# Optimization experiments

Measured on AMD Instinct MI355X. Metric: run time of the kernel, lower is better.

The kernel has to match this reference:

```python
import jax, jax.numpy as jnp
import numpy as np

B, L, D = 2, 4096, 768
H, HD = 12, 64
EPS = 1e-6


def setup_inputs() -> dict:
    key = jax.random.key(0)
    ks = jax.random.split(key, 5)
    x = jax.random.normal(ks[0], (B, L, D), dtype=jnp.float32)
    # realistic rope tables
    inv_freq = 1.0 / (10000.0 ** (np.arange(0, HD, 2, dtype=np.float32) / HD))
    t = np.arange(L, dtype=np.float32)
    freqs = np.outer(t, inv_freq)  # (L, HD/2)
    emb = np.concatenate([freqs, freqs], axis=-1)  # (L, HD)
    rope_cos = jnp.asarray(np.cos(emb))
    rope_sin = jnp.asarray(np.sin(emb))
    Wqkv = jax.random.normal(ks[1], (3 * D, D), dtype=jnp.float32) * (1.0 / np.sqrt(D))
    Wout = jax.random.normal(ks[2], (D, D), dtype=jnp.float32) * (1.0 / np.sqrt(D))
    q_norm_w = jnp.ones((HD,), dtype=jnp.float32)
    k_norm_w = jnp.ones((HD,), dtype=jnp.float32)
    return {"x": x, "rope_cos": rope_cos, "rope_sin": rope_sin,
            "Wqkv": Wqkv, "Wout": Wout,
            "q_norm_w": q_norm_w, "k_norm_w": k_norm_w}


def _rms_norm(x, w):
    # x: (..., HD); computed in float32 like the torch module
    norm = jax.lax.rsqrt(jnp.mean(jnp.square(x.astype(jnp.float32)), axis=-1, keepdims=True) + EPS)
    return (x.astype(jnp.float32) * norm).astype(x.dtype) * w


def _rotate_half(x):
    x1, x2 = jnp.split(x, 2, axis=-1)
    return jnp.concatenate([-x2, x1], axis=-1)


def reference(x, rope_cos, rope_sin, Wqkv, Wout, q_norm_w, k_norm_w):
    b, l, d = x.shape
    # fused QKV projection (Linear with no bias): x @ Wqkv.T
    qkv = jnp.einsum('bld,ed->ble', x, Wqkv).reshape(b, l, 3, H, HD)
    q, k, v = qkv[:, :, 0], qkv[:, :, 1], qkv[:, :, 2]  # (B, L, H, HD)
    q = jnp.transpose(q, (0, 2, 1, 3))  # (B, H, L, HD)
    k = jnp.transpose(k, (0, 2, 1, 3))
    v = jnp.transpose(v, (0, 2, 1, 3))
    # per-head RMSNorm on q and k
    q = _rms_norm(q, q_norm_w)
    k = _rms_norm(k, k_norm_w)
    # RoPE: cos/sin (L, HD) broadcast over (B, H)
    cos = rope_cos[None, None, :, :]
    sin = rope_sin[None, None, :, :]
    q = q * cos + _rotate_half(q) * sin
    k = k * cos + _rotate_half(k) * sin
    # scaled dot product attention (no mask)
    scale = 1.0 / jnp.sqrt(jnp.asarray(HD, dtype=q.dtype))
    scores = jnp.einsum('bhqd,bhkd->bhqk', q, k) * scale  # (B, H, L, L)
    attn = jax.nn.softmax(scores, axis=-1)
    out = jnp.einsum('bhqk,bhkd->bhqd', attn, v)  # (B, H, L, HD)
    out = jnp.transpose(out, (0, 2, 1, 3)).reshape(b, l, d)
    return jnp.einsum('bld,ed->ble', out, Wout)
```

## Files before the change

### kernel.cpp

```cpp
#include <hip/hip_runtime.h>
#include <hip/hip_bf16.h>

typedef float f32x4 __attribute__((ext_vector_type(4)));
typedef float f32x16 __attribute__((ext_vector_type(16)));
typedef short bf16x8 __attribute__((ext_vector_type(8)));
typedef unsigned short ushort8_t __attribute__((ext_vector_type(8)));

#define L_SEQ 4096
#define DMODEL 768
#define NHEAD 12
#define HDIM 64
#define QSCALE (0.125f * 1.44269504f)

__device__ __forceinline__ unsigned short f2bf(float f) {
    __hip_bfloat16 h = __float2bfloat16(f);
    return *reinterpret_cast<unsigned short*>(&h);
}

__device__ __forceinline__ unsigned pack2bf(float a, float b) {
    return (unsigned)f2bf(a) | ((unsigned)f2bf(b) << 16);
}

__device__ __forceinline__ void gload16(const void* g, void* l) {
    __builtin_amdgcn_global_load_lds(
        (const __attribute__((address_space(1))) unsigned int*)g,
        (__attribute__((address_space(3))) unsigned int*)l, 16, 0, 0);
}

__global__ __launch_bounds__(256) void cvt3_f32_bf16(
    const float* __restrict__ a, unsigned short* __restrict__ oa, int na,
    const float* __restrict__ bsrc, unsigned short* __restrict__ ob, int nb,
    const float* __restrict__ csrc, unsigned short* __restrict__ oc, int nc)
{
    int i = (blockIdx.x * 256 + threadIdx.x) * 4;
    const float* in; unsigned short* out;
    if (i < na) { in = a; out = oa; }
    else if (i < na + nb) { in = bsrc; out = ob; i -= na; }
    else if (i < na + nb + nc) { in = csrc; out = oc; i -= na + nb; }
    else return;
    float4 v = *reinterpret_cast<const float4*>(in + i);
    ushort4 o;
    o.x = f2bf(v.x); o.y = f2bf(v.y); o.z = f2bf(v.z); o.w = f2bf(v.w);
    *reinterpret_cast<ushort4*>(out + i) = o;
}

#define BM 128
#define BN 128
#define BKK 64

__global__ __launch_bounds__(256) void gemm_qkv_fused(
    const unsigned short* __restrict__ A, const unsigned short* __restrict__ Bt,
    const float* __restrict__ cosb, const float* __restrict__ sinb,
    const float* __restrict__ qw, const float* __restrict__ kw,
    unsigned short* __restrict__ Qb, unsigned short* __restrict__ Kb,
    unsigned short* __restrict__ Vt)
{
    __shared__ union SM {
        struct { unsigned short As[BM][BKK]; unsigned short Bs[BN][BKK]; } st;
        unsigned short ep[4][64][72];
    } sm;

    const int K = DMODEL;
    const int tid  = threadIdx.x;
    const int lane = tid & 63;
    const int wid  = tid >> 6;
    const int r = lane & 15, g = lane >> 4;
    const int wr = wid >> 1, wc = wid & 1;
    const int m0 = blockIdx.y * BM;
    const int n0 = blockIdx.x * BN;

    f32x4 acc[4][4];
    for (int i = 0; i < 4; ++i)
        for (int j = 0; j < 4; ++j)
            acc[i][j] = (f32x4){0.f, 0.f, 0.f, 0.f};

    for (int kt = 0; kt < K; kt += BKK) {
        __syncthreads();
        for (int p = 0; p < 4; ++p) {
            int idx = wid * 64 + p * 256 + lane;
            int row = idx >> 3;
            int ch  = (idx & 7) * 8;
            gload16(&A[(size_t)(m0 + row) * K + kt + ch],
                    (char*)sm.st.As + (size_t)(wid * 64 + p * 256) * 16);
            gload16(&Bt[(size_t)(n0 + row) * K + kt + ch],
                    (char*)sm.st.Bs + (size_t)(wid * 64 + p * 256) * 16);
        }
        __syncthreads();
        for (int k0 = 0; k0 < BKK; k0 += 32) {
            bf16x8 a[4], b[4];
            for (int i = 0; i < 4; ++i)
                a[i] = *reinterpret_cast<const bf16x8*>(&sm.st.As[wr * 64 + i * 16 + r][k0 + 8 * g]);
            for (int j = 0; j < 4; ++j)
                b[j] = *reinterpret_cast<const bf16x8*>(&sm.st.Bs[wc * 64 + j * 16 + r][k0 + 8 * g]);
            for (int i = 0; i < 4; ++i)
                for (int j = 0; j < 4; ++j)
                    acc[i][j] = __builtin_amdgcn_mfma_f32_16x16x32_bf16(a[i], b[j], acc[i][j], 0, 0, 0);
        }
    }

    __syncthreads();

    const int e0  = n0 + wc * 64;
    const int sec = e0 / DMODEL;
    const int h   = (e0 % DMODEL) / HDIM;
    const int row0 = m0 + wr * 64;
    const int b   = row0 >> 12;
    const int l0  = row0 & (L_SEQ - 1);
    unsigned short (*ep)[72] = sm.ep[wid];

    if (sec < 2) {
        const float* nw = (sec == 0) ? qw : kw;
        float wv[4];
        for (int j = 0; j < 4; ++j) wv[j] = nw[j * 16 + r];
        for (int i = 0; i < 4; ++i) {
            for (int t = 0; t < 4; ++t) {
                float ss = acc[i][0][t] * acc[i][0][t] + acc[i][1][t] * acc[i][1][t]
                         + acc[i][2][t] * acc[i][2][t] + acc[i][3][t] * acc[i][3][t];
                ss += __shfl_xor(ss, 1);
                ss += __shfl_xor(ss, 2);
                ss += __shfl_xor(ss, 4);
                ss += __shfl_xor(ss, 8);
                float inv = rsqrtf(ss * (1.f / 64.f) + 1e-6f);
                int lr = i * 16 + 4 * g + t;
                int l  = l0 + lr;
                float qn[4];
                for (int j = 0; j < 4; ++j) qn[j] = acc[i][j][t] * inv * wv[j];
                for (int j = 0; j < 4; ++j) {
                    int d = j * 16 + r;
                    float c = cosb[l * HDIM + d], s = sinb[l * HDIM + d];
                    float sgn = (j < 2) ? -1.f : 1.f;
                    float res = qn[j] * c + sgn * qn[j ^ 2] * s;
                    if (sec == 0) res *= QSCALE;
                    ep[lr][d] = f2bf(res);
                }
            }
        }
        unsigned short* dst = ((sec == 0) ? Qb : Kb)
            + ((size_t)(b * NHEAD + h) * L_SEQ + l0) * HDIM;
        for (int it = 0; it < 8; ++it) {
            int idx = it * 64 + lane;
            int lr = idx >> 3, ch = (idx & 7) * 8;
            ushort8_t v = *reinterpret_cast<const ushort8_t*>(&ep[lr][ch]);
            *reinterpret_cast<ushort8_t*>(&dst[(size_t)lr * HDIM + ch]) = v;
        }
    } else {
        for (int i = 0; i < 4; ++i)
            for (int t = 0; t < 4; ++t) {
                int lr = i * 16 + 4 * g + t;
                for (int j = 0; j < 4; ++j)
                    ep[j * 16 + r][lr] = f2bf(acc[i][j][t]);
            }
        unsigned short* dst = Vt + ((size_t)(b * NHEAD + h) * HDIM) * L_SEQ + l0;
        for (int it = 0; it < 8; ++it) {
            int idx = it * 64 + lane;
            int d = idx >> 3, ch = (idx & 7) * 8;
            ushort8_t v = *reinterpret_cast<const ushort8_t*>(&ep[d][ch]);
            *reinterpret_cast<ushort8_t*>(&dst[(size_t)d * L_SEQ + ch]) = v;
        }
    }
}

__global__ __launch_bounds__(256) void gemm_bf16_nt(
    const unsigned short* __restrict__ A, const unsigned short* __restrict__ Bt,
    float* __restrict__ C, int M, int N, int K)
{
    __shared__ unsigned short As[BM][BKK];
    __shared__ unsigned short Bs[BN][BKK];
    const int tid  = threadIdx.x;
    const int lane = tid & 63;
    const int wid  = tid >> 6;
    const int r = lane & 15, g = lane >> 4;
    const int wr = wid >> 1, wc = wid & 1;
    const int m0 = blockIdx.y * BM;
    const int n0 = blockIdx.x * BN;

    f32x4 acc[4][4];
    for (int i = 0; i < 4; ++i)
        for (int j = 0; j < 4; ++j)
            acc[i][j] = (f32x4){0.f, 0.f, 0.f, 0.f};

    for (int kt = 0; kt < K; kt += BKK) {
        __syncthreads();
        for (int p = 0; p < 4; ++p) {
            int idx = wid * 64 + p * 256 + lane;
            int row = idx >> 3;
            int ch  = (idx & 7) * 8;
            gload16(&A[(size_t)(m0 + row) * K + kt + ch],
                    (char*)As + (size_t)(wid * 64 + p * 256) * 16);
            gload16(&Bt[(size_t)(n0 + row) * K + kt + ch],
                    (char*)Bs + (size_t)(wid * 64 + p * 256) * 16);
        }
        __syncthreads();
        for (int k0 = 0; k0 < BKK; k0 += 32) {
            bf16x8 a[4], b[4];
            for (int i = 0; i < 4; ++i)
                a[i] = *reinterpret_cast<const bf16x8*>(&As[wr * 64 + i * 16 + r][k0 + 8 * g]);
            for (int j = 0; j < 4; ++j)
                b[j] = *reinterpret_cast<const bf16x8*>(&Bs[wc * 64 + j * 16 + r][k0 + 8 * g]);
            for (int i = 0; i < 4; ++i)
                for (int j = 0; j < 4; ++j)
                    acc[i][j] = __builtin_amdgcn_mfma_f32_16x16x32_bf16(a[i], b[j], acc[i][j], 0, 0, 0);
        }
    }
    for (int i = 0; i < 4; ++i)
        for (int j = 0; j < 4; ++j)
            for (int t = 0; t < 4; ++t) {
                int row = m0 + wr * 64 + i * 16 + 4 * g + t;
                int col = n0 + wc * 64 + j * 16 + r;
                C[(size_t)row * N + col] = acc[i][j][t];
            }
}

__global__ __launch_bounds__(256, 3) void flashattn(
    const unsigned short* __restrict__ Qb, const unsigned short* __restrict__ Kb,
    const unsigned short* __restrict__ Vt, unsigned short* __restrict__ aob)
{
    __shared__ unsigned short Ksm[2][64 * 64];
    __shared__ unsigned short Vsm[2][64 * 64];

    const int lin = blockIdx.x;
    const int bh = (lin & 7) + 8 * (lin >> 8);
    const int qblk = (lin >> 3) & 31;
    const int b = bh / NHEAD, h = bh % NHEAD;
    const int tid = threadIdx.x;
    const int wid = tid >> 6, lane = tid & 63;
    const int l31 = lane & 31, half = lane >> 5;
    const int q0 = qblk * 128 + wid * 32;

    bf16x8 qf[4];
    {
        const unsigned short* Qp = Qb + ((size_t)bh * L_SEQ + q0 + l31) * HDIM + 8 * half;
        for (int dt = 0; dt < 4; ++dt)
            qf[dt] = *reinterpret_cast<const bf16x8*>(Qp + dt * 16);
    }

    bf16x8 onesf;
    for (int e = 0; e < 8; ++e) onesf[e] = (l31 == 0) ? (short)0x3F80 : (short)0;

    const unsigned short* Kbase = Kb + (size_t)bh * L_SEQ * HDIM;
    const unsigned short* Vbase = Vt + (size_t)bh * HDIM * L_SEQ;

    const int idx0 = tid, idx1 = tid + 256;
    const int row0 = idx0 >> 3, row1 = idx1 >> 3;
    const int c0 = ((idx0 & 7) * 16) ^ ((row0 & 7) << 4);
    const int c1 = ((idx1 & 7) * 16) ^ ((row1 & 7) << 4);
    const char* kp0 = (const char*)(Kbase + (size_t)row0 * HDIM) + c0;
    const char* kp1 = (const char*)(Kbase + (size_t)row1 * HDIM) + c1;
    const char* vp0 = (const char*)(Vbase + (size_t)row0 * L_SEQ) + c0;
    const char* vp1 = (const char*)(Vbase + (size_t)row1 * L_SEQ) + c1;

    f32x16 o0, o1, o_l, sA0, sA1, sB0, sB1;
    for (int e = 0; e < 16; ++e) {
        o0[e] = 0.f; o1[e] = 0.f; o_l[e] = 0.f;
        sA0[e] = 0.f; sA1[e] = 0.f; sB0[e] = 0.f; sB1[e] = 0.f;
    }

    auto stageK = [&](int buf, int t) {
        size_t off = (size_t)t * (64 * HDIM * 2);
        gload16(kp0 + off, (char*)Ksm[buf] + wid * 1024);
        gload16(kp1 + off, (char*)Ksm[buf] + wid * 1024 + 4096);
    };
    auto stageV = [&](int buf, int t) {
        size_t off = (size_t)t * 128;
        gload16(vp0 + off, (char*)Vsm[buf] + wid * 1024);
        gload16(vp1 + off, (char*)Vsm[buf] + wid * 1024 + 4096);
    };

    auto qk = [&](f32x16& s0, f32x16& s1, const unsigned short* Kbuf) {
        const char* rp0 = (const char*)Kbuf + l31 * 128;
        const char* rp1 = rp0 + 32 * 128;
        const int sw = (l31 & 7) << 4;
        for (int dt = 0; dt < 4; ++dt) {
            int co = (dt * 32 + half * 16) ^ sw;
            bf16x8 kf0 = *reinterpret_cast<const bf16x8*>(rp0 + co);
            bf16x8 kf1 = *reinterpret_cast<const bf16x8*>(rp1 + co);
            s0 = __builtin_amdgcn_mfma_f32_32x32x16_bf16(kf0, qf[dt], s0, 0, 0, 0);
            s1 = __builtin_amdgcn_mfma_f32_32x32x16_bf16(kf1, qf[dt], s1, 0, 0, 0);
        }
    };

    auto softmax_pa = [&](f32x16& s0, f32x16& s1, bf16x8* pa) {
        for (int kh = 0; kh < 2; ++kh) {
            f32x16& s = kh ? s1 : s0;
            float p[16];
            for (int e = 0; e < 16; ++e) p[e] = __builtin_amdgcn_exp2f(s[e]);
            for (int kk = 0; kk < 2; ++kk) {
                unsigned A = pack2bf(p[8 * kk + 0], p[8 * kk + 1]);
                unsigned Bp = pack2bf(p[8 * kk + 2], p[8 * kk + 3]);
                unsigned C = pack2bf(p[8 * kk + 4], p[8 * kk + 5]);
                unsigned D = pack2bf(p[8 * kk + 6], p[8 * kk + 7]);
                asm("v_permlane32_swap_b32 %0, %1" : "+v"(A), "+v"(C));
                asm("v_permlane32_swap_b32 %0, %1" : "+v"(Bp), "+v"(D));
                union { unsigned u[4]; bf16x8 v; } tt;
                tt.u[0] = A; tt.u[1] = Bp; tt.u[2] = C; tt.u[3] = D;
                pa[2 * kh + kk] = tt.v;
            }
            for (int e = 0; e < 16; ++e) s[e] = 0.f;
        }
    };

    auto pv = [&](const bf16x8* pa, const unsigned short* Vbuf) {
        for (int kt = 0; kt < 4; ++kt)
            o_l = __builtin_amdgcn_mfma_f32_32x32x16_bf16(pa[kt], onesf, o_l, 0, 0, 0);
        const char* rp0 = (const char*)Vbuf + l31 * 128;
        const char* rp1 = rp0 + 32 * 128;
        const int sw = (l31 & 7) << 4;
        for (int kt = 0; kt < 4; ++kt) {
            int co = (kt * 32 + half * 16) ^ sw;
            bf16x8 vf0 = *reinterpret_cast<const bf16x8*>(rp0 + co);
            bf16x8 vf1 = *reinterpret_cast<const bf16x8*>(rp1 + co);
            o0 = __builtin_amdgcn_mfma_f32_32x32x16_bf16(pa[kt], vf0, o0, 0, 0, 0);
            o1 = __builtin_amdgcn_mfma_f32_32x32x16_bf16(pa[kt], vf1, o1, 0, 0, 0);
        }
    };

    stageK(0, 0);
    __syncthreads();
    stageK(1, 1); stageV(0, 0);
    __builtin_amdgcn_s_setprio(1);
    qk(sA0, sA1, Ksm[0]);
    __builtin_amdgcn_s_setprio(0);
    __syncthreads();

    bf16x8 pa[4];
    for (int i = 0; i < 31; ++i) {
        int t1 = 2 * i + 1;
        stageK(0, t1 + 1); stageV(1, t1);
        __builtin_amdgcn_s_setprio(1);
        qk(sB0, sB1, Ksm[1]);
        softmax_pa(sA0, sA1, pa);
        pv(pa, Vsm[0]);
        __builtin_amdgcn_s_setprio(0);
        __syncthreads();
        int t2 = t1 + 1;
        stageK(1, t2 + 1); stageV(0, t2);
        __builtin_amdgcn_s_setprio(1);
        qk(sA0, sA1, Ksm[0]);
        softmax_pa(sB0, sB1, pa);
        pv(pa, Vsm[1]);
        __builtin_amdgcn_s_setprio(0);
        __syncthreads();
    }
    stageV(1, 63);
    __builtin_amdgcn_s_setprio(1);
    qk(sB0, sB1, Ksm[1]);
    softmax_pa(sA0, sA1, pa);
    pv(pa, Vsm[0]);
    __builtin_amdgcn_s_setprio(0);
    __syncthreads();
    softmax_pa(sB0, sB1, pa);
    pv(pa, Vsm[1]);

    float linv[16];
    for (int j = 0; j < 16; ++j)
        linv[j] = 1.f / __shfl(o_l[j], lane & 32);
    for (int j = 0; j < 16; ++j) {
        int q = (j & 3) + 8 * (j >> 2) + 4 * half;
        size_t base = ((size_t)(b * L_SEQ + q0 + q)) * DMODEL + h * HDIM + l31;
        aob[base] = f2bf(o0[j] * linv[j]);
        aob[base + 32] = f2bf(o1[j] * linv[j]);
    }
}

extern "C" void kernel_launch(void* const* d_in, const int* in_sizes, int n_in,
                              void* d_out, int out_size, void* d_ws, size_t ws_size,
                              hipStream_t stream) {
    const float* x        = (const float*)d_in[0];
    const float* rope_cos = (const float*)d_in[1];
    const float* rope_sin = (const float*)d_in[2];
    const float* Wqkv     = (const float*)d_in[3];
    const float* Wout     = (const float*)d_in[4];
    const float* q_norm_w = (const float*)d_in[5];
    const float* k_norm_w = (const float*)d_in[6];
    float* out = (float*)d_out;

    const int BL = 2 * L_SEQ;
    const int nx    = BL * DMODEL;
    const int nwqkv = 3 * DMODEL * DMODEL;
    const int nwout = DMODEL * DMODEL;

    char* w = (char*)d_ws;
    unsigned short* xb    = (unsigned short*)w; w += (size_t)nx * 2;
    unsigned short* wqkvb = (unsigned short*)w; w += (size_t)nwqkv * 2;
    unsigned short* woutb = (unsigned short*)w; w += (size_t)nwout * 2;
    unsigned short* Qb    = (unsigned short*)w; w += (size_t)nx * 2;
    unsigned short* Kb    = (unsigned short*)w; w += (size_t)nx * 2;
    unsigned short* Vtb   = (unsigned short*)w; w += (size_t)nx * 2;
    unsigned short* aob   = (unsigned short*)w; w += (size_t)nx * 2;

    {
        int total = (nx + nwqkv + nwout) / 4;
        cvt3_f32_bf16<<<(total + 255) / 256, 256, 0, stream>>>(
            x, xb, nx, Wqkv, wqkvb, nwqkv, Wout, woutb, nwout);
    }

    {
        dim3 grid(3 * DMODEL / BN, BL / BM);
        gemm_qkv_fused<<<grid, 256, 0, stream>>>(xb, wqkvb, rope_cos, rope_sin,
                                                 q_norm_w, k_norm_w, Qb, Kb, Vtb);
    }

    flashattn<<<768, 256, 0, stream>>>(Qb, Kb, Vtb, aob);

    {
        dim3 grid(DMODEL / BN, BL / BM);
        gemm_bf16_nt<<<grid, 256, 0, stream>>>(aob, woutb, out, BL, DMODEL, DMODEL);
    }
}
```

Before: 222.8 us.

## Replace ping-pong QK/softmax pipeline with triple-buffered K/V ring

The attention main loop now uses a three-slot LDS ring for K and V tiles. Each iteration prefetches the next tile, waits on vmcnt so only the current tile's loads must be complete, and uses a single barrier per tile. This replaces the two-buffer scheme in which the QK product of the next tile was interleaved with softmax and PV of the current one. The aim is to cut barrier stalls and hide global load latency better. In exchange it gives up the overlap of MFMA work with the exp/pack work, raises LDS use from 32 KB to 48 KB per block, which may cost occupancy, and adds a redundant out-of-range prefetch on the final iteration.

```diff
diff --git a/kernel.cpp b/kernel.cpp
--- a/kernel.cpp
+++ b/kernel.cpp
@@ -215,8 +215,8 @@
     const unsigned short* __restrict__ Qb, const unsigned short* __restrict__ Kb,
     const unsigned short* __restrict__ Vt, unsigned short* __restrict__ aob)
 {
-    __shared__ unsigned short Ksm[2][64 * 64];
-    __shared__ unsigned short Vsm[2][64 * 64];
+    __shared__ unsigned short Ksm[3][64 * 64];
+    __shared__ unsigned short Vsm[3][64 * 64];
 
     const int lin = blockIdx.x;
     const int bh = (lin & 7) + 8 * (lin >> 8);
@@ -249,10 +249,9 @@
     const char* vp0 = (const char*)(Vbase + (size_t)row0 * L_SEQ) + c0;
     const char* vp1 = (const char*)(Vbase + (size_t)row1 * L_SEQ) + c1;
 
-    f32x16 o0, o1, o_l, sA0, sA1, sB0, sB1;
+    f32x16 o0, o1, o_l, s0, s1;
     for (int e = 0; e < 16; ++e) {
-        o0[e] = 0.f; o1[e] = 0.f; o_l[e] = 0.f;
-        sA0[e] = 0.f; sA1[e] = 0.f; sB0[e] = 0.f; sB1[e] = 0.f;
+        o0[e] = 0.f; o1[e] = 0.f; o_l[e] = 0.f; s0[e] = 0.f; s1[e] = 0.f;
     }
 
     auto stageK = [&](int buf, int t) {
@@ -266,20 +265,34 @@
         gload16(vp1 + off, (char*)Vsm[buf] + wid * 1024 + 4096);
     };
 
-    auto qk = [&](f32x16& s0, f32x16& s1, const unsigned short* Kbuf) {
-        const char* rp0 = (const char*)Kbuf + l31 * 128;
-        const char* rp1 = rp0 + 32 * 128;
-        const int sw = (l31 & 7) << 4;
-        for (int dt = 0; dt < 4; ++dt) {
-            int co = (dt * 32 + half * 16) ^ sw;
-            bf16x8 kf0 = *reinterpret_cast<const bf16x8*>(rp0 + co);
-            bf16x8 kf1 = *reinterpret_cast<const bf16x8*>(rp1 + co);
-            s0 = __builtin_amdgcn_mfma_f32_32x32x16_bf16(kf0, qf[dt], s0, 0, 0, 0);
-            s1 = __builtin_amdgcn_mfma_f32_32x32x16_bf16(kf1, qf[dt], s1, 0, 0, 0);
-        }
-    };
-
-    auto softmax_pa = [&](f32x16& s0, f32x16& s1, bf16x8* pa) {
+    stageK(0, 0); stageV(0, 0);
+    int cur = 0, nxt = 1;
+
+    bf16x8 pa[4];
+    for (int t = 0; t < 64; ++t) {
+        stageK(nxt, t + 1); stageV(nxt, t + 1);
+        asm volatile("s_waitcnt vmcnt(4)" ::: "memory");
+        __builtin_amdgcn_s_barrier();
+        __builtin_amdgcn_sched_barrier(0);
+
+        const char* KsB = (const char*)Ksm[cur];
+        const char* VsB = (const char*)Vsm[cur];
+
+        __builtin_amdgcn_s_setprio(1);
+        {
+            const char* rp0 = KsB + l31 * 128;
+            const char* rp1 = rp0 + 32 * 128;
+            const int sw = (l31 & 7) << 4;
+            for (int dt = 0; dt < 4; ++dt) {
+                int co = (dt * 32 + half * 16) ^ sw;
+                bf16x8 kf0 = *reinterpret_cast<const bf16x8*>(rp0 + co);
+                bf16x8 kf1 = *reinterpret_cast<const bf16x8*>(rp1 + co);
+                s0 = __builtin_amdgcn_mfma_f32_32x32x16_bf16(kf0, qf[dt], s0, 0, 0, 0);
+                s1 = __builtin_amdgcn_mfma_f32_32x32x16_bf16(kf1, qf[dt], s1, 0, 0, 0);
+            }
+        }
+        __builtin_amdgcn_s_setprio(0);
+
         for (int kh = 0; kh < 2; ++kh) {
             f32x16& s = kh ? s1 : s0;
             float p[16];
@@ -297,59 +310,27 @@
             }
             for (int e = 0; e < 16; ++e) s[e] = 0.f;
         }
-    };
-
-    auto pv = [&](const bf16x8* pa, const unsigned short* Vbuf) {
+
+        __builtin_amdgcn_s_setprio(1);
         for (int kt = 0; kt < 4; ++kt)
             o_l = __builtin_amdgcn_mfma_f32_32x32x16_bf16(pa[kt], onesf, o_l, 0, 0, 0);
-        const char* rp0 = (const char*)Vbuf + l31 * 128;
-        const char* rp1 = rp0 + 32 * 128;
-        const int sw = (l31 & 7) << 4;
-        for (int kt = 0; kt < 4; ++kt) {
-            int co = (kt * 32 + half * 16) ^ sw;
-            bf16x8 vf0 = *reinterpret_cast<const bf16x8*>(rp0 + co);
-            bf16x8 vf1 = *reinterpret_cast<const bf16x8*>(rp1 + co);
-            o0 = __builtin_amdgcn_mfma_f32_32x32x16_bf16(pa[kt], vf0, o0, 0, 0, 0);
-            o1 = __builtin_amdgcn_mfma_f32_32x32x16_bf16(pa[kt], vf1, o1, 0, 0, 0);
-        }
-    };
-
-    stageK(0, 0);
-    __syncthreads();
-    stageK(1, 1); stageV(0, 0);
-    __builtin_amdgcn_s_setprio(1);
-    qk(sA0, sA1, Ksm[0]);
-    __builtin_amdgcn_s_setprio(0);
-    __syncthreads();
-
-    bf16x8 pa[4];
-    for (int i = 0; i < 31; ++i) {
-        int t1 = 2 * i + 1;
-        stageK(0, t1 + 1); stageV(1, t1);
-        __builtin_amdgcn_s_setprio(1);
-        qk(sB0, sB1, Ksm[1]);
-        softmax_pa(sA0, sA1, pa);
-        pv(pa, Vsm[0]);
+        {
+            const char* rp0 = VsB + l31 * 128;
+            const char* rp1 = rp0 + 32 * 128;
+            const int sw = (l31 & 7) << 4;
+            for (int kt = 0; kt < 4; ++kt) {
+                int co = (kt * 32 + half * 16) ^ sw;
+                bf16x8 vf0 = *reinterpret_cast<const bf16x8*>(rp0 + co);
+                bf16x8 vf1 = *reinterpret_cast<const bf16x8*>(rp1 + co);
+                o0 = __builtin_amdgcn_mfma_f32_32x32x16_bf16(pa[kt], vf0, o0, 0, 0, 0);
+                o1 = __builtin_amdgcn_mfma_f32_32x32x16_bf16(pa[kt], vf1, o1, 0, 0, 0);
+            }
+        }
         __builtin_amdgcn_s_setprio(0);
-        __syncthreads();
-        int t2 = t1 + 1;
-        stageK(1, t2 + 1); stageV(0, t2);
-        __builtin_amdgcn_s_setprio(1);
-        qk(sA0, sA1, Ksm[0]);
-        softmax_pa(sB0, sB1, pa);
-        pv(pa, Vsm[1]);
-        __builtin_amdgcn_s_setprio(0);
-        __syncthreads();
-    }
-    stageV(1, 63);
-    __builtin_amdgcn_s_setprio(1);
-    qk(sB0, sB1, Ksm[1]);
-    softmax_pa(sA0, sA1, pa);
-    pv(pa, Vsm[0]);
-    __builtin_amdgcn_s_setprio(0);
-    __syncthreads();
-    softmax_pa(sB0, sB1, pa);
-    pv(pa, Vsm[1]);
+
+        cur = nxt;
+        nxt = (nxt == 2) ? 0 : nxt + 1;
+    }
 
     float linv[16];
     for (int j = 0; j < 16; ++j)
```

Result: no change. 226.9 us (+1.9%).
